# Kernel tuning notes

Hardware: AMD Instinct MI355X
Metric: run time of the kernel (lower is better)

## Reference

```python
import jax, jax.numpy as jnp
import numpy as np

N_ITERATIONS = 3
BN_EPS = 1e-5


def _conv2d(x, w, b, pad):
    # x: [N,C,H,W], w: [O,I,kh,kw] (OIHW)
    y = jax.lax.conv_general_dilated(
        x, w, window_strides=(1, 1), padding=[(pad, pad), (pad, pad)],
        dimension_numbers=("NCHW", "OIHW", "NCHW"))
    return y + b[None, :, None, None]


def setup_inputs() -> dict:
    key = jax.random.key(0)
    S, B, C, H, W = 4, 4, 64, 32, 32
    ks = jax.random.split(key, 12)
    rn = lambda k, shape, s=0.05: jax.random.normal(k, shape, jnp.float32) * s
    f32 = jnp.float32
    return {
        "x": jax.random.normal(ks[0], (S, B, C, H, W), f32),
        "Wf_w": rn(ks[1], (C, C, 3, 3)), "Wf_b": jnp.zeros((C,), f32),
        "Wh_w": rn(ks[2], (C, C, 3, 3)), "Wh_b": jnp.zeros((C,), f32),
        "Wl_w": rn(ks[3], (C, C, 3, 3)), "Wl_b": jnp.zeros((C,), f32),
        "alpha": jnp.ones((1,), f32),
        "Wc": rn(ks[4], (C, C), 0.02),
        "Wg_w": rn(ks[5], (C, C, 3, 3)), "Wg_b": jnp.zeros((C,), f32),
        "bn_gamma": jnp.ones((C,), f32), "bn_beta": jnp.zeros((C,), f32),
        "bn_mean": jnp.zeros((C,), f32), "bn_var": jnp.ones((C,), f32),
        "gru_zr_w": rn(ks[6], (2 * C, 2 * C, 5, 5)), "gru_zr_b": jnp.zeros((2 * C,), f32),
        "gru_h_w": rn(ks[7], (C, 2 * C, 5, 5)), "gru_h_b": jnp.zeros((C,), f32),
        "intra_w": jnp.float32(0.5), "inter_w": jnp.float32(0.5),
    }


def reference(x, Wf_w, Wf_b, Wh_w, Wh_b, Wl_w, Wl_b, alpha, Wc, Wg_w, Wg_b,
              bn_gamma, bn_beta, bn_mean, bn_var,
              gru_zr_w, gru_zr_b, gru_h_w, gru_h_b, intra_w, inter_w):
    S, B, C, H, W = x.shape
    HW = H * W
    pair_mask = (1.0 - jnp.eye(S, dtype=x.dtype))[:, :, None, None, None, None]
    h = x
    for _ in range(N_ITERATIONS):
        hm = h.reshape(S * B, C, H, W)
        # ---- intra attention (vectorized over S*B) ----
        ft = _conv2d(hm, Wf_w, Wf_b, 1).reshape(S, B, C, HW)
        ht = _conv2d(hm, Wh_w, Wh_b, 1).reshape(S, B, C, HW)
        lt = _conv2d(hm, Wl_w, Wl_b, 1).reshape(S, B, C, HW)
        attn = jax.nn.softmax(jnp.einsum("sbcm,sbcn->sbmn", ft, ht), axis=-1)
        ctx = jnp.einsum("sbmn,sbcn->sbcm", attn, lt).reshape(S, B, C, H, W)
        intra = alpha[0] * ctx + h
        # ---- inter attention over all (i, j) pairs ----
        hf = h.reshape(S, B, C, HW)
        yt = jnp.einsum("cd,jbdn->jbcn", Wc, hf)
        eij = jnp.einsum("ibcm,jbcn->ijbmn", hf, yt)  # [S,S,B,HW,HW]
        a = jax.nn.softmax(eij, axis=-1)
        mji = jnp.einsum("ijbmn,jbcn->ijbcm", a, hf)  # message to i from j
        g_in = mji.reshape(S * S * B, C, H, W)
        gji = jax.nn.sigmoid(jnp.mean(_conv2d(g_in, Wg_w, Wg_b, 1), axis=(2, 3), keepdims=True))
        mg = gji * g_in
        # BatchNorm2d (eval mode)
        mg = (mg - bn_mean[None, :, None, None]) / jnp.sqrt(bn_var[None, :, None, None] + BN_EPS)
        mg = mg * bn_gamma[None, :, None, None] + bn_beta[None, :, None, None]
        mg = mg.reshape(S, S, B, C, H, W)
        inter = jnp.sum(mg * pair_mask, axis=1)  # sum over j != i
        agg = intra_w * intra + inter_w * inter
        # ---- ConvGRU update (vectorized over S*B) + residual ----
        xg = agg.reshape(S * B, C, H, W)
        hg = h.reshape(S * B, C, H, W)
        zr = jax.nn.sigmoid(_conv2d(jnp.concatenate([xg, hg], axis=1), gru_zr_w, gru_zr_b, 2))
        z, r = zr[:, :C], zr[:, C:]
        h_hat = jnp.tanh(_conv2d(jnp.concatenate([xg, r * hg], axis=1), gru_h_w, gru_h_b, 2))
        h_new = (1.0 - z) * hg + z * h_hat
        h = (h_new + hg).reshape(S, B, C, H, W)
    return h
```

## Files before the change

kernel.cpp:

```cpp
#include <hip/hip_runtime.h>
#include <math.h>

#define SS 4
#define BB 4
#define CC 64
#define HH 32
#define WW 32
#define HWD 1024
#define CHW (CC*HWD)
#define NIMG (SS*BB)

__global__ __launch_bounds__(256) void conv3_triple_kernel(
    const float* __restrict__ h,
    const float* __restrict__ wf, const float* __restrict__ bf,
    const float* __restrict__ wh, const float* __restrict__ bh,
    const float* __restrict__ wl, const float* __restrict__ bl,
    float* __restrict__ ft, float* __restrict__ ht, float* __restrict__ lt)
{
    int img = blockIdx.x;
    int co  = blockIdx.y;
    __shared__ float tile[34*34];
    int tid = threadIdx.x;
    float accf[4] = {0,0,0,0}, acch[4] = {0,0,0,0}, accl[4] = {0,0,0,0};
    int px0 = tid * 4;
    int oy = px0 >> 5;
    int ox = px0 & 31;
    const float* hin = h + (size_t)img * CHW;
    for (int ci = 0; ci < CC; ++ci) {
        __syncthreads();
        for (int idx = tid; idx < 34*34; idx += 256) {
            int r = idx / 34 - 1, c = idx % 34 - 1;
            float v = 0.f;
            if ((unsigned)r < 32u && (unsigned)c < 32u) v = hin[ci*HWD + r*WW + c];
            tile[idx] = v;
        }
        __syncthreads();
        const float* pwf = wf + (co*CC + ci)*9;
        const float* pwh = wh + (co*CC + ci)*9;
        const float* pwl = wl + (co*CC + ci)*9;
        float wfv[9], whv[9], wlv[9];
        #pragma unroll
        for (int k = 0; k < 9; ++k) { wfv[k]=pwf[k]; whv[k]=pwh[k]; wlv[k]=pwl[k]; }
        #pragma unroll
        for (int dy = 0; dy < 3; ++dy) {
            const float* trow = &tile[(oy+dy)*34 + ox];
            float in[6];
            #pragma unroll
            for (int q = 0; q < 6; ++q) in[q] = trow[q];
            #pragma unroll
            for (int dx = 0; dx < 3; ++dx) {
                float a = wfv[dy*3+dx], b = whv[dy*3+dx], c = wlv[dy*3+dx];
                #pragma unroll
                for (int p = 0; p < 4; ++p) {
                    accf[p] += a * in[dx+p];
                    acch[p] += b * in[dx+p];
                    accl[p] += c * in[dx+p];
                }
            }
        }
    }
    float bfv = bf[co], bhv = bh[co], blv = bl[co];
    size_t out = (size_t)img*CHW + co*HWD + px0;
    #pragma unroll
    for (int p = 0; p < 4; ++p) {
        ft[out+p] = accf[p] + bfv;
        ht[out+p] = acch[p] + bhv;
        lt[out+p] = accl[p] + blv;
    }
}

__device__ __forceinline__ void flash_core(
    const float* __restrict__ Q, const float* __restrict__ K,
    const float* __restrict__ V, float* __restrict__ O, int m0)
{
    __shared__ float kt[64*65];
    __shared__ float vt[64*65];
    int tid = threadIdx.x;
    int ml = tid >> 2;
    int cq = tid & 3;
    int m = m0 + ml;
    float q[16];
    #pragma unroll
    for (int k = 0; k < 16; ++k) q[k] = Q[(cq*16+k)*HWD + m];
    float acc[16];
    #pragma unroll
    for (int k = 0; k < 16; ++k) acc[k] = 0.f;
    float mx = -3.0e38f, l = 0.f;

    for (int nt = 0; nt < 16; ++nt) {
        int n0 = nt * 64;
        __syncthreads();
        for (int idx = tid; idx < 64*64; idx += 256) {
            int r = idx >> 6, c = idx & 63;
            kt[r*65+c] = K[r*HWD + n0 + c];
            vt[r*65+c] = V[r*HWD + n0 + c];
        }
        __syncthreads();
        float s[64];
        #pragma unroll
        for (int n = 0; n < 64; ++n) {
            float a = 0.f;
            #pragma unroll
            for (int k = 0; k < 16; ++k) a += q[k] * kt[(cq*16+k)*65 + n];
            s[n] = a;
        }
        #pragma unroll
        for (int n = 0; n < 64; ++n) {
            s[n] += __shfl_xor(s[n], 1);
            s[n] += __shfl_xor(s[n], 2);
        }
        float tm = s[0];
        #pragma unroll
        for (int n = 1; n < 64; ++n) tm = fmaxf(tm, s[n]);
        float nmx = fmaxf(mx, tm);
        float sc = __expf(mx - nmx);
        float ts = 0.f;
        #pragma unroll
        for (int n = 0; n < 64; ++n) { s[n] = __expf(s[n] - nmx); ts += s[n]; }
        l = l * sc + ts;
        mx = nmx;
        #pragma unroll
        for (int k = 0; k < 16; ++k) {
            float a = acc[k] * sc;
            #pragma unroll
            for (int n = 0; n < 64; ++n) a += s[n] * vt[(cq*16+k)*65 + n];
            acc[k] = a;
        }
    }
    float inv = 1.f / l;
    #pragma unroll
    for (int k = 0; k < 16; ++k) O[(cq*16+k)*HWD + m] = acc[k] * inv;
}

__global__ __launch_bounds__(256) void flash_intra_kernel(
    const float* __restrict__ ft, const float* __restrict__ ht,
    const float* __restrict__ lt, float* __restrict__ ctx)
{
    int inst = blockIdx.y;
    int m0 = blockIdx.x * 64;
    flash_core(ft + (size_t)inst*CHW, ht + (size_t)inst*CHW,
               lt + (size_t)inst*CHW, ctx + (size_t)inst*CHW, m0);
}

__global__ __launch_bounds__(256) void flash_inter_kernel(
    const float* __restrict__ h, const float* __restrict__ yt,
    float* __restrict__ mji, int j)
{
    int inst = blockIdx.y;
    int b = inst & 3;
    int m0 = blockIdx.x * 64;
    flash_core(h + (size_t)inst*CHW, yt + (size_t)(j*BB+b)*CHW,
               h + (size_t)(j*BB+b)*CHW, mji + (size_t)inst*CHW, m0);
}

__global__ __launch_bounds__(256) void yt_kernel(
    const float* __restrict__ Wc, const float* __restrict__ h,
    float* __restrict__ yt)
{
    int img = blockIdx.x;
    int n0 = blockIdx.y * 128;
    __shared__ float wc[64*64];
    __shared__ float hs[64*128];
    int tid = threadIdx.x;
    for (int i = tid; i < 4096; i += 256) wc[i] = Wc[i];
    for (int i = tid; i < 64*128; i += 256) {
        int d = i >> 7, n = i & 127;
        hs[i] = h[(size_t)img*CHW + d*HWD + n0 + n];
    }
    __syncthreads();
    int n = tid & 127;
    int c0 = (tid >> 7) * 32;
    for (int c = c0; c < c0+32; ++c) {
        float a = 0.f;
        #pragma unroll 8
        for (int d = 0; d < 64; ++d) a += wc[c*64+d] * hs[d*128+n];
        yt[(size_t)img*CHW + c*HWD + n0 + n] = a;
    }
}

__global__ __launch_bounds__(64) void gate_stats_kernel(
    const float* __restrict__ mji, float* __restrict__ stats)
{
    int img = blockIdx.x >> 6;
    int ci  = blockIdx.x & 63;
    const float* p = mji + ((size_t)img*CC + ci)*HWD;
    int l = threadIdx.x;
    float full=0, top=0, bot=0, left=0, right=0;
    #pragma unroll
    for (int k = 0; k < 16; ++k) {
        int px = l + 64*k;
        float v = p[px];
        int y = px >> 5, x = px & 31;
        full += v;
        if (y == 0)  top += v;
        if (y == 31) bot += v;
        if (x == 0)  left += v;
        if (x == 31) right += v;
    }
    #pragma unroll
    for (int msk = 1; msk < 64; msk <<= 1) {
        full  += __shfl_xor(full,  msk);
        top   += __shfl_xor(top,   msk);
        bot   += __shfl_xor(bot,   msk);
        left  += __shfl_xor(left,  msk);
        right += __shfl_xor(right, msk);
    }
    if (l == 0) {
        float* o = stats + ((size_t)img*CC + ci)*9;
        o[0]=full; o[1]=top; o[2]=bot; o[3]=left; o[4]=right;
        o[5]=p[0]; o[6]=p[31]; o[7]=p[992]; o[8]=p[1023];
    }
}

__global__ __launch_bounds__(64) void gate_gji_kernel(
    const float* __restrict__ stats, const float* __restrict__ wg,
    const float* __restrict__ bg, float* __restrict__ gji)
{
    int img = blockIdx.x;
    int o = threadIdx.x;
    float acc = 0.f;
    for (int ci = 0; ci < CC; ++ci) {
        const float* st = stats + ((size_t)img*CC + ci)*9;
        float F=st[0], T=st[1], Bo=st[2], L=st[3], R=st[4];
        float TL=st[5], TR=st[6], BL=st[7], BR=st[8];
        const float* w = wg + (o*CC + ci)*9;
        float S00 = F - Bo - R + BR;
        float S01 = F - Bo;
        float S02 = F - Bo - L + BL;
        float S10 = F - R;
        float S11 = F;
        float S12 = F - L;
        float S20 = F - T - R + TR;
        float S21 = F - T;
        float S22 = F - T - L + TL;
        acc += w[0]*S00 + w[1]*S01 + w[2]*S02
             + w[3]*S10 + w[4]*S11 + w[5]*S12
             + w[6]*S20 + w[7]*S21 + w[8]*S22;
    }
    float m = acc * (1.f/1024.f) + bg[o];
    gji[img*CC + o] = 1.f / (1.f + __expf(-m));
}

__global__ __launch_bounds__(256) void inter_accum_kernel(
    const float* __restrict__ mji, const float* __restrict__ gji,
    float* __restrict__ acc, int j, int init)
{
    int idx = blockIdx.x * 256 + threadIdx.x;
    int iimg = idx >> 16;
    int c = (idx >> 10) & 63;
    int i = iimg >> 2;
    float v = (j != i) ? gji[iimg*CC + c] * mji[idx] : 0.f;
    if (init) acc[idx] = v; else acc[idx] += v;
}

__global__ __launch_bounds__(256) void agg_kernel(
    const float* __restrict__ ctx, const float* __restrict__ h,
    const float* __restrict__ acc, const float* __restrict__ alpha,
    const float* __restrict__ bn_gamma, const float* __restrict__ bn_beta,
    const float* __restrict__ bn_mean, const float* __restrict__ bn_var,
    const float* __restrict__ intra_w, const float* __restrict__ inter_w,
    float* __restrict__ agg)
{
    int idx = blockIdx.x * 256 + threadIdx.x;
    int c = (idx >> 10) & 63;
    float scale = bn_gamma[c] / sqrtf(bn_var[c] + 1e-5f);
    float cst = 3.f * (bn_beta[c] - bn_mean[c]*scale);
    float intra = alpha[0]*ctx[idx] + h[idx];
    float inter = scale*acc[idx] + cst;
    agg[idx] = intra_w[0]*intra + inter_w[0]*inter;
}

__global__ __launch_bounds__(256) void conv5_zr_kernel(
    const float* __restrict__ agg, const float* __restrict__ h,
    const float* __restrict__ w, const float* __restrict__ bias,
    float* __restrict__ zr)
{
    int img = blockIdx.x;
    int co  = blockIdx.y;
    __shared__ float tile[36*36];
    int tid = threadIdx.x;
    float acc[4] = {0,0,0,0};
    int px0 = tid * 4;
    int oy = px0 >> 5, ox = px0 & 31;
    for (int ci = 0; ci < 128; ++ci) {
        const float* src = (ci < 64) ? (agg + (size_t)img*CHW + ci*HWD)
                                     : (h + (size_t)img*CHW + (ci-64)*HWD);
        __syncthreads();
        for (int idx = tid; idx < 36*36; idx += 256) {
            int r = idx / 36 - 2, c = idx % 36 - 2;
            float v = 0.f;
            if ((unsigned)r < 32u && (unsigned)c < 32u) v = src[r*WW + c];
            tile[idx] = v;
        }
        __syncthreads();
        const float* pw = w + (co*128 + ci)*25;
        float wv[25];
        #pragma unroll
        for (int k = 0; k < 25; ++k) wv[k] = pw[k];
        #pragma unroll
        for (int dy = 0; dy < 5; ++dy) {
            const float* trow = &tile[(oy+dy)*36 + ox];
            float in[8];
            #pragma unroll
            for (int q = 0; q < 8; ++q) in[q] = trow[q];
            #pragma unroll
            for (int dx = 0; dx < 5; ++dx) {
                float wk = wv[dy*5+dx];
                #pragma unroll
                for (int p = 0; p < 4; ++p) acc[p] += wk * in[dx+p];
            }
        }
    }
    float bv = bias[co];
    size_t out = (size_t)img*128*HWD + co*HWD + px0;
    #pragma unroll
    for (int p = 0; p < 4; ++p)
        zr[out+p] = 1.f / (1.f + __expf(-(acc[p] + bv)));
}

__global__ __launch_bounds__(256) void conv5_hh_kernel(
    const float* __restrict__ agg, const float* __restrict__ h,
    const float* __restrict__ zr, const float* __restrict__ w,
    const float* __restrict__ bias, float* __restrict__ hh)
{
    int img = blockIdx.x;
    int co  = blockIdx.y;
    __shared__ float tile[36*36];
    int tid = threadIdx.x;
    float acc[4] = {0,0,0,0};
    int px0 = tid * 4;
    int oy = px0 >> 5, ox = px0 & 31;
    for (int ci = 0; ci < 128; ++ci) {
        __syncthreads();
        if (ci < 64) {
            const float* src = agg + (size_t)img*CHW + ci*HWD;
            for (int idx = tid; idx < 36*36; idx += 256) {
                int r = idx / 36 - 2, c = idx % 36 - 2;
                float v = 0.f;
                if ((unsigned)r < 32u && (unsigned)c < 32u) v = src[r*WW + c];
                tile[idx] = v;
            }
        } else {
            const float* srcH = h + (size_t)img*CHW + (ci-64)*HWD;
            const float* srcR = zr + (size_t)img*128*HWD + ci*HWD;
            for (int idx = tid; idx < 36*36; idx += 256) {
                int r = idx / 36 - 2, c = idx % 36 - 2;
                float v = 0.f;
                if ((unsigned)r < 32u && (unsigned)c < 32u) v = srcH[r*WW + c] * srcR[r*WW + c];
                tile[idx] = v;
            }
        }
        __syncthreads();
        const float* pw = w + (co*128 + ci)*25;
        float wv[25];
        #pragma unroll
        for (int k = 0; k < 25; ++k) wv[k] = pw[k];
        #pragma unroll
        for (int dy = 0; dy < 5; ++dy) {
            const float* trow = &tile[(oy+dy)*36 + ox];
            float in[8];
            #pragma unroll
            for (int q = 0; q < 8; ++q) in[q] = trow[q];
            #pragma unroll
            for (int dx = 0; dx < 5; ++dx) {
                float wk = wv[dy*5+dx];
                #pragma unroll
                for (int p = 0; p < 4; ++p) acc[p] += wk * in[dx+p];
            }
        }
    }
    float bv = bias[co];
    size_t out = (size_t)img*CHW + co*HWD + px0;
    #pragma unroll
    for (int p = 0; p < 4; ++p) hh[out+p] = tanhf(acc[p] + bv);
}

__global__ __launch_bounds__(256) void gru_update_kernel(
    const float* __restrict__ zr, const float* __restrict__ hh,
    float* __restrict__ h)
{
    int idx = blockIdx.x * 256 + threadIdx.x;
    int img = idx >> 16;
    int rem = idx & 65535;
    float z = zr[(size_t)img*131072 + rem];
    float hv = h[idx], hhv = hh[idx];
    h[idx] = (2.f - z) * hv + z * hhv;
}

extern "C" void kernel_launch(void* const* d_in, const int* in_sizes, int n_in,
                              void* d_out, int out_size, void* d_ws, size_t ws_size,
                              hipStream_t stream)
{
    const float* x        = (const float*)d_in[0];
    const float* Wf_w     = (const float*)d_in[1];
    const float* Wf_b     = (const float*)d_in[2];
    const float* Wh_w     = (const float*)d_in[3];
    const float* Wh_b     = (const float*)d_in[4];
    const float* Wl_w     = (const float*)d_in[5];
    const float* Wl_b     = (const float*)d_in[6];
    const float* alpha    = (const float*)d_in[7];
    const float* Wc       = (const float*)d_in[8];
    const float* Wg_w     = (const float*)d_in[9];
    const float* Wg_b     = (const float*)d_in[10];
    const float* bn_gamma = (const float*)d_in[11];
    const float* bn_beta  = (const float*)d_in[12];
    const float* bn_mean  = (const float*)d_in[13];
    const float* bn_var   = (const float*)d_in[14];
    const float* gru_zr_w = (const float*)d_in[15];
    const float* gru_zr_b = (const float*)d_in[16];
    const float* gru_h_w  = (const float*)d_in[17];
    const float* gru_h_b  = (const float*)d_in[18];
    const float* intra_w  = (const float*)d_in[19];
    const float* inter_w  = (const float*)d_in[20];

    float* h  = (float*)d_out;
    float* ws = (float*)d_ws;
    const size_t M = 1048576;
    float* ft    = ws;
    float* ht_   = ws + 1*M;
    float* lt    = ws + 2*M;
    float* ctx   = ws + 3*M;
    float* yt    = ws + 4*M;
    float* mji   = ws + 5*M;
    float* iacc  = ws + 6*M;
    float* stats = ws + 7*M;
    float* gji   = stats + 16384;
    float* agg   = ft;
    float* zr    = ht_;
    float* hh    = yt;

    hipMemcpyAsync(h, x, M * sizeof(float), hipMemcpyDeviceToDevice, stream);

    for (int it = 0; it < 3; ++it) {
        conv3_triple_kernel<<<dim3(NIMG, CC), 256, 0, stream>>>(
            h, Wf_w, Wf_b, Wh_w, Wh_b, Wl_w, Wl_b, ft, ht_, lt);
        flash_intra_kernel<<<dim3(16, NIMG), 256, 0, stream>>>(ft, ht_, lt, ctx);
        yt_kernel<<<dim3(NIMG, 8), 256, 0, stream>>>(Wc, h, yt);
        for (int j = 0; j < SS; ++j) {
            flash_inter_kernel<<<dim3(16, NIMG), 256, 0, stream>>>(h, yt, mji, j);
            gate_stats_kernel<<<1024, 64, 0, stream>>>(mji, stats);
            gate_gji_kernel<<<16, 64, 0, stream>>>(stats, Wg_w, Wg_b, gji);
            inter_accum_kernel<<<4096, 256, 0, stream>>>(mji, gji, iacc, j, j == 0 ? 1 : 0);
        }
        agg_kernel<<<4096, 256, 0, stream>>>(ctx, h, iacc, alpha,
            bn_gamma, bn_beta, bn_mean, bn_var, intra_w, inter_w, agg);
        conv5_zr_kernel<<<dim3(NIMG, 128), 256, 0, stream>>>(agg, h, gru_zr_w, gru_zr_b, zr);
        conv5_hh_kernel<<<dim3(NIMG, 64), 256, 0, stream>>>(agg, h, zr, gru_h_w, gru_h_b, hh);
        gru_update_kernel<<<4096, 256, 0, stream>>>(zr, hh, h);
    }
}
```

Before: 9.173 ms.

## Batch all flash attention instances into one launch and vectorize conv/flash loads

Result: faster. 7.395 ms (-19.4%).

```diff
diff --git a/kernel.cpp b/kernel.cpp
--- a/kernel.cpp
+++ b/kernel.cpp
@@ -4,8 +4,6 @@
 #define SS 4
 #define BB 4
 #define CC 64
-#define HH 32
-#define WW 32
 #define HWD 1024
 #define CHW (CC*HWD)
 #define NIMG (SS*BB)
@@ -19,20 +17,22 @@
 {
     int img = blockIdx.x;
     int co  = blockIdx.y;
-    __shared__ float tile[34*34];
+    __shared__ __align__(16) float tile[34*36];
     int tid = threadIdx.x;
     float accf[4] = {0,0,0,0}, acch[4] = {0,0,0,0}, accl[4] = {0,0,0,0};
     int px0 = tid * 4;
     int oy = px0 >> 5;
     int ox = px0 & 31;
     const float* hin = h + (size_t)img * CHW;
+    for (int idx = tid; idx < 34*36; idx += 256) tile[idx] = 0.f;
+    int sr = tid >> 3;
+    int sc = (tid & 7) * 4;
     for (int ci = 0; ci < CC; ++ci) {
         __syncthreads();
-        for (int idx = tid; idx < 34*34; idx += 256) {
-            int r = idx / 34 - 1, c = idx % 34 - 1;
-            float v = 0.f;
-            if ((unsigned)r < 32u && (unsigned)c < 32u) v = hin[ci*HWD + r*WW + c];
-            tile[idx] = v;
+        {
+            float4 v = *(const float4*)(hin + ci*HWD + sr*32 + sc);
+            float* dst = &tile[(sr+1)*36 + 1 + sc];
+            dst[0]=v.x; dst[1]=v.y; dst[2]=v.z; dst[3]=v.w;
         }
         __syncthreads();
         const float* pwf = wf + (co*CC + ci)*9;
@@ -43,10 +43,10 @@
         for (int k = 0; k < 9; ++k) { wfv[k]=pwf[k]; whv[k]=pwh[k]; wlv[k]=pwl[k]; }
         #pragma unroll
         for (int dy = 0; dy < 3; ++dy) {
-            const float* trow = &tile[(oy+dy)*34 + ox];
-            float in[6];
-            #pragma unroll
-            for (int q = 0; q < 6; ++q) in[q] = trow[q];
+            const float* trow = &tile[(oy+dy)*36 + ox];
+            float4 a4 = *(const float4*)trow;
+            float2 b2 = *(const float2*)(trow + 4);
+            float in[6] = {a4.x, a4.y, a4.z, a4.w, b2.x, b2.y};
             #pragma unroll
             for (int dx = 0; dx < 3; ++dx) {
                 float a = wfv[dy*3+dx], b = whv[dy*3+dx], c = wlv[dy*3+dx];
@@ -61,24 +61,22 @@
     }
     float bfv = bf[co], bhv = bh[co], blv = bl[co];
     size_t out = (size_t)img*CHW + co*HWD + px0;
-    #pragma unroll
-    for (int p = 0; p < 4; ++p) {
-        ft[out+p] = accf[p] + bfv;
-        ht[out+p] = acch[p] + bhv;
-        lt[out+p] = accl[p] + blv;
-    }
+    float4 rf = {accf[0]+bfv, accf[1]+bfv, accf[2]+bfv, accf[3]+bfv};
+    float4 rh = {acch[0]+bhv, acch[1]+bhv, acch[2]+bhv, acch[3]+bhv};
+    float4 rl = {accl[0]+blv, accl[1]+blv, accl[2]+blv, accl[3]+blv};
+    *(float4*)(ft + out) = rf;
+    *(float4*)(ht + out) = rh;
+    *(float4*)(lt + out) = rl;
 }
 
 __device__ __forceinline__ void flash_core(
     const float* __restrict__ Q, const float* __restrict__ K,
-    const float* __restrict__ V, float* __restrict__ O, int m0)
-{
-    __shared__ float kt[64*65];
-    __shared__ float vt[64*65];
+    const float* __restrict__ V, float* __restrict__ O, int m0,
+    float4* kt4, float4* vt4)
+{
     int tid = threadIdx.x;
-    int ml = tid >> 2;
     int cq = tid & 3;
-    int m = m0 + ml;
+    int m = m0 + (tid >> 2);
     float q[16];
     #pragma unroll
     for (int k = 0; k < 16; ++k) q[k] = Q[(cq*16+k)*HWD + m];
@@ -90,40 +88,60 @@
     for (int nt = 0; nt < 16; ++nt) {
         int n0 = nt * 64;
         __syncthreads();
-        for (int idx = tid; idx < 64*64; idx += 256) {
-            int r = idx >> 6, c = idx & 63;
-            kt[r*65+c] = K[r*HWD + n0 + c];
-            vt[r*65+c] = V[r*HWD + n0 + c];
-        }
-        __syncthreads();
-        float s[64];
-        #pragma unroll
-        for (int n = 0; n < 64; ++n) {
-            float a = 0.f;
+        #pragma unroll
+        for (int t = 0; t < 4; ++t) {
+            int u = tid + t*256;
+            int r = u >> 4, c4 = u & 15;
+            int p = c4 ^ ((r >> 4) & 3);
+            kt4[r*17 + p] = *(const float4*)(K + r*HWD + n0 + c4*4);
+            vt4[r*17 + p] = *(const float4*)(V + r*HWD + n0 + c4*4);
+        }
+        __syncthreads();
+        float4 s4[16];
+        #pragma unroll
+        for (int nb = 0; nb < 16; ++nb) { s4[nb].x=0.f; s4[nb].y=0.f; s4[nb].z=0.f; s4[nb].w=0.f; }
+        #pragma unroll
+        for (int k = 0; k < 16; ++k) {
+            const float4* kr = &kt4[(cq*16+k)*17];
+            float qk = q[k];
             #pragma unroll
-            for (int k = 0; k < 16; ++k) a += q[k] * kt[(cq*16+k)*65 + n];
-            s[n] = a;
-        }
-        #pragma unroll
-        for (int n = 0; n < 64; ++n) {
-            s[n] += __shfl_xor(s[n], 1);
-            s[n] += __shfl_xor(s[n], 2);
-        }
-        float tm = s[0];
-        #pragma unroll
-        for (int n = 1; n < 64; ++n) tm = fmaxf(tm, s[n]);
+            for (int nb = 0; nb < 16; ++nb) {
+                float4 kv = kr[nb ^ cq];
+                s4[nb].x += qk*kv.x; s4[nb].y += qk*kv.y;
+                s4[nb].z += qk*kv.z; s4[nb].w += qk*kv.w;
+            }
+        }
+        #pragma unroll
+        for (int nb = 0; nb < 16; ++nb) {
+            s4[nb].x += __shfl_xor(s4[nb].x, 1); s4[nb].x += __shfl_xor(s4[nb].x, 2);
+            s4[nb].y += __shfl_xor(s4[nb].y, 1); s4[nb].y += __shfl_xor(s4[nb].y, 2);
+            s4[nb].z += __shfl_xor(s4[nb].z, 1); s4[nb].z += __shfl_xor(s4[nb].z, 2);
+            s4[nb].w += __shfl_xor(s4[nb].w, 1); s4[nb].w += __shfl_xor(s4[nb].w, 2);
+        }
+        float tm = -3.0e38f;
+        #pragma unroll
+        for (int nb = 0; nb < 16; ++nb)
+            tm = fmaxf(tm, fmaxf(fmaxf(s4[nb].x, s4[nb].y), fmaxf(s4[nb].z, s4[nb].w)));
         float nmx = fmaxf(mx, tm);
         float sc = __expf(mx - nmx);
         float ts = 0.f;
         #pragma unroll
-        for (int n = 0; n < 64; ++n) { s[n] = __expf(s[n] - nmx); ts += s[n]; }
+        for (int nb = 0; nb < 16; ++nb) {
+            s4[nb].x = __expf(s4[nb].x - nmx); s4[nb].y = __expf(s4[nb].y - nmx);
+            s4[nb].z = __expf(s4[nb].z - nmx); s4[nb].w = __expf(s4[nb].w - nmx);
+            ts += s4[nb].x + s4[nb].y + s4[nb].z + s4[nb].w;
+        }
         l = l * sc + ts;
         mx = nmx;
         #pragma unroll
         for (int k = 0; k < 16; ++k) {
+            const float4* vr = &vt4[(cq*16+k)*17];
             float a = acc[k] * sc;
             #pragma unroll
-            for (int n = 0; n < 64; ++n) a += s[n] * vt[(cq*16+k)*65 + n];
+            for (int nb = 0; nb < 16; ++nb) {
+                float4 vv = vr[nb ^ cq];
+                a += s4[nb].x*vv.x + s4[nb].y*vv.y + s4[nb].z*vv.z + s4[nb].w*vv.w;
+            }
             acc[k] = a;
         }
     }
@@ -132,25 +150,26 @@
     for (int k = 0; k < 16; ++k) O[(cq*16+k)*HWD + m] = acc[k] * inv;
 }
 
-__global__ __launch_bounds__(256) void flash_intra_kernel(
+__global__ __launch_bounds__(256) void flash_all_kernel(
+    const float* __restrict__ h, const float* __restrict__ yt,
     const float* __restrict__ ft, const float* __restrict__ ht,
-    const float* __restrict__ lt, float* __restrict__ ctx)
-{
+    const float* __restrict__ lt, float* __restrict__ ctx,
+    float* __restrict__ mji, int zbase)
+{
+    __shared__ __align__(16) float4 kt4[64*17];
+    __shared__ __align__(16) float4 vt4[64*17];
+    int z = zbase + blockIdx.z;
     int inst = blockIdx.y;
     int m0 = blockIdx.x * 64;
-    flash_core(ft + (size_t)inst*CHW, ht + (size_t)inst*CHW,
-               lt + (size_t)inst*CHW, ctx + (size_t)inst*CHW, m0);
-}
-
-__global__ __launch_bounds__(256) void flash_inter_kernel(
-    const float* __restrict__ h, const float* __restrict__ yt,
-    float* __restrict__ mji, int j)
-{
-    int inst = blockIdx.y;
-    int b = inst & 3;
-    int m0 = blockIdx.x * 64;
-    flash_core(h + (size_t)inst*CHW, yt + (size_t)(j*BB+b)*CHW,
-               h + (size_t)(j*BB+b)*CHW, mji + (size_t)inst*CHW, m0);
+    if (z < 4) {
+        int b = inst & 3;
+        int slot = blockIdx.z * 16 + inst;
+        flash_core(h + (size_t)inst*CHW, yt + (size_t)(z*BB+b)*CHW,
+                   h + (size_t)(z*BB+b)*CHW, mji + (size_t)slot*CHW, m0, kt4, vt4);
+    } else {
+        flash_core(ft + (size_t)inst*CHW, ht + (size_t)inst*CHW,
+                   lt + (size_t)inst*CHW, ctx + (size_t)inst*CHW, m0, kt4, vt4);
+    }
 }
 
 __global__ __launch_bounds__(256) void yt_kernel(
@@ -181,9 +200,9 @@
 __global__ __launch_bounds__(64) void gate_stats_kernel(
     const float* __restrict__ mji, float* __restrict__ stats)
 {
-    int img = blockIdx.x >> 6;
-    int ci  = blockIdx.x & 63;
-    const float* p = mji + ((size_t)img*CC + ci)*HWD;
+    int slot = blockIdx.x >> 6;
+    int ci   = blockIdx.x & 63;
+    const float* p = mji + ((size_t)slot*CC + ci)*HWD;
     int l = threadIdx.x;
     float full=0, top=0, bot=0, left=0, right=0;
     #pragma unroll
@@ -206,7 +225,7 @@
         right += __shfl_xor(right, msk);
     }
     if (l == 0) {
-        float* o = stats + ((size_t)img*CC + ci)*9;
+        float* o = stats + ((size_t)slot*CC + ci)*9;
         o[0]=full; o[1]=top; o[2]=bot; o[3]=left; o[4]=right;
         o[5]=p[0]; o[6]=p[31]; o[7]=p[992]; o[8]=p[1023];
     }
@@ -216,29 +235,54 @@
     const float* __restrict__ stats, const float* __restrict__ wg,
     const float* __restrict__ bg, float* __restrict__ gji)
 {
-    int img = blockIdx.x;
+    int slot = blockIdx.x;
     int o = threadIdx.x;
     float acc = 0.f;
     for (int ci = 0; ci < CC; ++ci) {
-        const float* st = stats + ((size_t)img*CC + ci)*9;
+        const float* st = stats + ((size_t)slot*CC + ci)*9;
         float F=st[0], T=st[1], Bo=st[2], L=st[3], R=st[4];
         float TL=st[5], TR=st[6], BL=st[7], BR=st[8];
         const float* w = wg + (o*CC + ci)*9;
-        float S00 = F - Bo - R + BR;
-        float S01 = F - Bo;
-        float S02 = F - Bo - L + BL;
-        float S10 = F - R;
-        float S11 = F;
-        float S12 = F - L;
-        float S20 = F - T - R + TR;
-        float S21 = F - T;
-        float S22 = F - T - L + TL;
-        acc += w[0]*S00 + w[1]*S01 + w[2]*S02
-             + w[3]*S10 + w[4]*S11 + w[5]*S12
-             + w[6]*S20 + w[7]*S21 + w[8]*S22;
-    }
-    float m = acc * (1.f/1024.f) + bg[o];
-    gji[img*CC + o] = 1.f / (1.f + __expf(-m));
+        acc += w[0]*(F-Bo-R+BR) + w[1]*(F-Bo) + w[2]*(F-Bo-L+BL)
+             + w[3]*(F-R)       + w[4]*F      + w[5]*(F-L)
+             + w[6]*(F-T-R+TR)  + w[7]*(F-T)  + w[8]*(F-T-L+TL);
+    }
+    float mv = acc * (1.f/1024.f) + bg[o];
+    gji[slot*CC + o] = 1.f / (1.f + __expf(-mv));
+}
+
+__global__ __launch_bounds__(256) void agg_fused_kernel(
+    const float* __restrict__ ctx, const float* __restrict__ h,
+    const float* __restrict__ mji, const float* __restrict__ gji,
+    const float* __restrict__ alpha,
+    const float* __restrict__ bn_gamma, const float* __restrict__ bn_beta,
+    const float* __restrict__ bn_mean, const float* __restrict__ bn_var,
+    const float* __restrict__ intra_w, const float* __restrict__ inter_w,
+    float* __restrict__ agg)
+{
+    int u = blockIdx.x * 256 + threadIdx.x;
+    int idx = u * 4;
+    int img = idx >> 16;
+    int c = (idx >> 10) & 63;
+    int i = img >> 2;
+    float4 s = {0,0,0,0};
+    #pragma unroll
+    for (int j = 0; j < 4; ++j) {
+        float g = (j != i) ? gji[(j*16+img)*CC + c] : 0.f;
+        float4 mv = *(const float4*)(mji + (size_t)(j*16+img)*CHW + (idx & 65535));
+        s.x += g*mv.x; s.y += g*mv.y; s.z += g*mv.z; s.w += g*mv.w;
+    }
+    float scale = bn_gamma[c] / sqrtf(bn_var[c] + 1e-5f);
+    float cst = 3.f * (bn_beta[c] - bn_mean[c]*scale);
+    float4 cv = *(const float4*)(ctx + idx);
+    float4 hv = *(const float4*)(h + idx);
+    float al = alpha[0], iw = intra_w[0], ew = inter_w[0];
+    float4 o;
+    o.x = iw*(al*cv.x + hv.x) + ew*(scale*s.x + cst);
+    o.y = iw*(al*cv.y + hv.y) + ew*(scale*s.y + cst);
+    o.z = iw*(al*cv.z + hv.z) + ew*(scale*s.z + cst);
+    o.w = iw*(al*cv.w + hv.w) + ew*(scale*s.w + cst);
+    *(float4*)(agg + idx) = o;
 }
 
 __global__ __launch_bounds__(256) void inter_accum_kernel(
@@ -277,20 +321,24 @@
 {
     int img = blockIdx.x;
     int co  = blockIdx.y;
-    __shared__ float tile[36*36];
+    __shared__ __align__(16) float tile[36*36];
     int tid = threadIdx.x;
     float acc[4] = {0,0,0,0};
     int px0 = tid * 4;
     int oy = px0 >> 5, ox = px0 & 31;
+    int sr = tid >> 3;
+    int sc = (tid & 7) * 4;
+    for (int idx = tid; idx < 36*36; idx += 256) tile[idx] = 0.f;
     for (int ci = 0; ci < 128; ++ci) {
         const float* src = (ci < 64) ? (agg + (size_t)img*CHW + ci*HWD)
                                      : (h + (size_t)img*CHW + (ci-64)*HWD);
         __syncthreads();
-        for (int idx = tid; idx < 36*36; idx += 256) {
-            int r = idx / 36 - 2, c = idx % 36 - 2;
-            float v = 0.f;
-            if ((unsigned)r < 32u && (unsigned)c < 32u) v = src[r*WW + c];
-            tile[idx] = v;
+        {
+            float4 v = *(const float4*)(src + sr*32 + sc);
+            float* dst = &tile[(sr+2)*36 + 2 + sc];
+            float2 lo = {v.x, v.y}, hi = {v.z, v.w};
+            *(float2*)dst = lo;
+            *(float2*)(dst+2) = hi;
         }
         __syncthreads();
         const float* pw = w + (co*128 + ci)*25;
@@ -300,9 +348,9 @@
         #pragma unroll
         for (int dy = 0; dy < 5; ++dy) {
             const float* trow = &tile[(oy+dy)*36 + ox];
-            float in[8];
-            #pragma unroll
-            for (int q = 0; q < 8; ++q) in[q] = trow[q];
+            float4 a4 = *(const float4*)trow;
+            float4 b4 = *(const float4*)(trow + 4);
+            float in[8] = {a4.x,a4.y,a4.z,a4.w,b4.x,b4.y,b4.z,b4.w};
             #pragma unroll
             for (int dx = 0; dx < 5; ++dx) {
                 float wk = wv[dy*5+dx];
@@ -313,9 +361,12 @@
     }
     float bv = bias[co];
     size_t out = (size_t)img*128*HWD + co*HWD + px0;
-    #pragma unroll
-    for (int p = 0; p < 4; ++p)
-        zr[out+p] = 1.f / (1.f + __expf(-(acc[p] + bv)));
+    float4 o;
+    o.x = 1.f/(1.f+__expf(-(acc[0]+bv)));
+    o.y = 1.f/(1.f+__expf(-(acc[1]+bv)));
+    o.z = 1.f/(1.f+__expf(-(acc[2]+bv)));
+    o.w = 1.f/(1.f+__expf(-(acc[3]+bv)));
+    *(float4*)(zr + out) = o;
 }
 
 __global__ __launch_bounds__(256) void conv5_hh_kernel(
@@ -325,30 +376,29 @@
 {
     int img = blockIdx.x;
     int co  = blockIdx.y;
-    __shared__ float tile[36*36];
+    __shared__ __align__(16) float tile[36*36];
     int tid = threadIdx.x;
     float acc[4] = {0,0,0,0};
     int px0 = tid * 4;
     int oy = px0 >> 5, ox = px0 & 31;
+    int sr = tid >> 3;
+    int sc = (tid & 7) * 4;
+    for (int idx = tid; idx < 36*36; idx += 256) tile[idx] = 0.f;
     for (int ci = 0; ci < 128; ++ci) {
         __syncthreads();
-        if (ci < 64) {
-            const float* src = agg + (size_t)img*CHW + ci*HWD;
-            for (int idx = tid; idx < 36*36; idx += 256) {
-                int r = idx / 36 - 2, c = idx % 36 - 2;
-                float v = 0.f;
-                if ((unsigned)r < 32u && (unsigned)c < 32u) v = src[r*WW + c];
-                tile[idx] = v;
-            }
-        } else {
-            const float* srcH = h + (size_t)img*CHW + (ci-64)*HWD;
-            const float* srcR = zr + (size_t)img*128*HWD + ci*HWD;
-            for (int idx = tid; idx < 36*36; idx += 256) {
-                int r = idx / 36 - 2, c = idx % 36 - 2;
-                float v = 0.f;
-                if ((unsigned)r < 32u && (unsigned)c < 32u) v = srcH[r*WW + c] * srcR[r*WW + c];
-                tile[idx] = v;
-            }
+        {
+            float4 v;
+            if (ci < 64) {
+                v = *(const float4*)(agg + (size_t)img*CHW + ci*HWD + sr*32 + sc);
+            } else {
+                float4 a = *(const float4*)(h + (size_t)img*CHW + (ci-64)*HWD + sr*32 + sc);
+                float4 b = *(const float4*)(zr + (size_t)img*128*HWD + ci*HWD + sr*32 + sc);
+                v.x = a.x*b.x; v.y = a.y*b.y; v.z = a.z*b.z; v.w = a.w*b.w;
+            }
+            float* dst = &tile[(sr+2)*36 + 2 + sc];
+            float2 lo = {v.x, v.y}, hi = {v.z, v.w};
+            *(float2*)dst = lo;
+            *(float2*)(dst+2) = hi;
         }
         __syncthreads();
         const float* pw = w + (co*128 + ci)*25;
@@ -358,9 +408,9 @@
         #pragma unroll
         for (int dy = 0; dy < 5; ++dy) {
             const float* trow = &tile[(oy+dy)*36 + ox];
-            float in[8];
-            #pragma unroll
-            for (int q = 0; q < 8; ++q) in[q] = trow[q];
+            float4 a4 = *(const float4*)trow;
+            float4 b4 = *(const float4*)(trow + 4);
+            float in[8] = {a4.x,a4.y,a4.z,a4.w,b4.x,b4.y,b4.z,b4.w};
             #pragma unroll
             for (int dx = 0; dx < 5; ++dx) {
                 float wk = wv[dy*5+dx];
@@ -371,20 +421,28 @@
     }
     float bv = bias[co];
     size_t out = (size_t)img*CHW + co*HWD + px0;
-    #pragma unroll
-    for (int p = 0; p < 4; ++p) hh[out+p] = tanhf(acc[p] + bv);
+    float4 o;
+    o.x = tanhf(acc[0]+bv); o.y = tanhf(acc[1]+bv);
+    o.z = tanhf(acc[2]+bv); o.w = tanhf(acc[3]+bv);
+    *(float4*)(hh + out) = o;
 }
 
 __global__ __launch_bounds__(256) void gru_update_kernel(
     const float* __restrict__ zr, const float* __restrict__ hh,
     float* __restrict__ h)
 {
-    int idx = blockIdx.x * 256 + threadIdx.x;
+    int idx = (blockIdx.x * 256 + threadIdx.x) * 4;
     int img = idx >> 16;
     int rem = idx & 65535;
-    float z = zr[(size_t)img*131072 + rem];
-    float hv = h[idx], hhv = hh[idx];
-    h[idx] = (2.f - z) * hv + z * hhv;
+    float4 z = *(const float4*)(zr + (size_t)img*131072 + rem);
+    float4 hv = *(const float4*)(h + idx);
+    float4 hhv = *(const float4*)(hh + idx);
+    float4 o;
+    o.x = (2.f-z.x)*hv.x + z.x*hhv.x;
+    o.y = (2.f-z.y)*hv.y + z.y*hhv.y;
+    o.z = (2.f-z.z)*hv.z + z.z*hhv.z;
+    o.w = (2.f-z.w)*hv.w + z.w*hhv.w;
+    *(float4*)(h + idx) = o;
 }
 
 extern "C" void kernel_launch(void* const* d_in, const int* in_sizes, int n_in,
@@ -416,36 +474,71 @@
     float* h  = (float*)d_out;
     float* ws = (float*)d_ws;
     const size_t M = 1048576;
-    float* ft    = ws;
-    float* ht_   = ws + 1*M;
-    float* lt    = ws + 2*M;
-    float* ctx   = ws + 3*M;
-    float* yt    = ws + 4*M;
-    float* mji   = ws + 5*M;
-    float* iacc  = ws + 6*M;
-    float* stats = ws + 7*M;
-    float* gji   = stats + 16384;
-    float* agg   = ft;
-    float* zr    = ht_;
-    float* hh    = yt;
 
     hipMemcpyAsync(h, x, M * sizeof(float), hipMemcpyDeviceToDevice, stream);
 
-    for (int it = 0; it < 3; ++it) {
-        conv3_triple_kernel<<<dim3(NIMG, CC), 256, 0, stream>>>(
-            h, Wf_w, Wf_b, Wh_w, Wh_b, Wl_w, Wl_b, ft, ht_, lt);
-        flash_intra_kernel<<<dim3(16, NIMG), 256, 0, stream>>>(ft, ht_, lt, ctx);
-        yt_kernel<<<dim3(NIMG, 8), 256, 0, stream>>>(Wc, h, yt);
-        for (int j = 0; j < SS; ++j) {
-            flash_inter_kernel<<<dim3(16, NIMG), 256, 0, stream>>>(h, yt, mji, j);
-            gate_stats_kernel<<<1024, 64, 0, stream>>>(mji, stats);
-            gate_gji_kernel<<<16, 64, 0, stream>>>(stats, Wg_w, Wg_b, gji);
-            inter_accum_kernel<<<4096, 256, 0, stream>>>(mji, gji, iacc, j, j == 0 ? 1 : 0);
-        }
-        agg_kernel<<<4096, 256, 0, stream>>>(ctx, h, iacc, alpha,
-            bn_gamma, bn_beta, bn_mean, bn_var, intra_w, inter_w, agg);
-        conv5_zr_kernel<<<dim3(NIMG, 128), 256, 0, stream>>>(agg, h, gru_zr_w, gru_zr_b, zr);
-        conv5_hh_kernel<<<dim3(NIMG, 64), 256, 0, stream>>>(agg, h, zr, gru_h_w, gru_h_b, hh);
-        gru_update_kernel<<<4096, 256, 0, stream>>>(zr, hh, h);
-    }
-}
+    const size_t NEED_BATCHED = (9*M + 64*64*9 + 64*64) * sizeof(float);
+    bool batched = (ws_size >= NEED_BATCHED);
+
+    if (batched) {
+        float* ft    = ws;
+        float* ht_   = ws + 1*M;
+        float* lt    = ws + 2*M;
+        float* ctx   = ws + 3*M;
+        float* yt    = ws + 4*M;
+        float* mji   = ws + 5*M;
+        float* stats = ws + 9*M;
+        float* gji   = stats + 64*64*9;
+        float* agg   = ft;
+        float* zr    = ht_;
+        float* hh    = yt;
+
+        for (int it = 0; it < 3; ++it) {
+            conv3_triple_kernel<<<dim3(NIMG, CC), 256, 0, stream>>>(
+                h, Wf_w, Wf_b, Wh_w, Wh_b, Wl_w, Wl_b, ft, ht_, lt);
+            yt_kernel<<<dim3(NIMG, 8), 256, 0, stream>>>(Wc, h, yt);
+            flash_all_kernel<<<dim3(16, NIMG, 5), 256, 0, stream>>>(
+                h, yt, ft, ht_, lt, ctx, mji, 0);
+            gate_stats_kernel<<<64*64, 64, 0, stream>>>(mji, stats);
+            gate_gji_kernel<<<64, 64, 0, stream>>>(stats, Wg_w, Wg_b, gji);
+            agg_fused_kernel<<<1024, 256, 0, stream>>>(ctx, h, mji, gji, alpha,
+                bn_gamma, bn_beta, bn_mean, bn_var, intra_w, inter_w, agg);
+            conv5_zr_kernel<<<dim3(NIMG, 128), 256, 0, stream>>>(agg, h, gru_zr_w, gru_zr_b, zr);
+            conv5_hh_kernel<<<dim3(NIMG, 64), 256, 0, stream>>>(agg, h, zr, gru_h_w, gru_h_b, hh);
+            gru_update_kernel<<<1024, 256, 0, stream>>>(zr, hh, h);
+        }
+    } else {
+        float* ft    = ws;
+        float* ht_   = ws + 1*M;
+        float* lt    = ws + 2*M;
+        float* ctx   = ws + 3*M;
+        float* yt    = ws + 4*M;
+        float* mji   = ws + 5*M;
+        float* iacc  = ws + 6*M;
+        float* stats = ws + 7*M;
+        float* gji   = stats + 16*64*9;
+        float* agg   = ft;
+        float* zr    = ht_;
+        float* hh    = yt;
+
+        for (int it = 0; it < 3; ++it) {
+            conv3_triple_kernel<<<dim3(NIMG, CC), 256, 0, stream>>>(
+                h, Wf_w, Wf_b, Wh_w, Wh_b, Wl_w, Wl_b, ft, ht_, lt);
+            yt_kernel<<<dim3(NIMG, 8), 256, 0, stream>>>(Wc, h, yt);
+            flash_all_kernel<<<dim3(16, NIMG, 1), 256, 0, stream>>>(
+                h, yt, ft, ht_, lt, ctx, mji, 4);
+            for (int j = 0; j < SS; ++j) {
+                flash_all_kernel<<<dim3(16, NIMG, 1), 256, 0, stream>>>(
+                    h, yt, ft, ht_, lt, ctx, mji, j);
+                gate_stats_kernel<<<16*64, 64, 0, stream>>>(mji, stats);
+                gate_gji_kernel<<<16, 64, 0, stream>>>(stats, Wg_w, Wg_b, gji);
+                inter_accum_kernel<<<4096, 256, 0, stream>>>(mji, gji, iacc, j, j == 0 ? 1 : 0);
+            }
+            agg_kernel<<<4096, 256, 0, stream>>>(ctx, h, iacc, alpha,
+                bn_gamma, bn_beta, bn_mean, bn_var, intra_w, inter_w, agg);
+            conv5_zr_kernel<<<dim3(NIMG, 128), 256, 0, stream>>>(agg, h, gru_zr_w, gru_zr_b, zr);
+            conv5_hh_kernel<<<dim3(NIMG, 64), 256, 0, stream>>>(agg, h, zr, gru_h_w, gru_h_b, hh);
+            gru_update_kernel<<<1024, 256, 0, stream>>>(zr, hh, h);
+        }
+    }
+}
```
